# Performance work log

Measured on AMD Instinct MI355X. Metric: run time of the kernel, lower is better.

The kernel has to match this reference:

```python
import jax, jax.numpy as jnp
import numpy as np

B, L, H = 16, 2048, 768
V, D = 30000, 64


def setup_inputs() -> dict:
    key = jax.random.key(0)
    k1, k2, k3, k4 = jax.random.split(key, 4)
    bert_x = jax.random.normal(k1, (B, L, H), dtype=jnp.float32)
    x = jax.random.randint(k2, (B, L), 0, V, dtype=jnp.int64)
    ae = jax.random.normal(k3, (V, D), dtype=jnp.float32)
    w = jax.random.normal(k4, (D, D), dtype=jnp.float32)
    return {"bert_x": bert_x, "x": x, "ae": ae, "w": w}


def reference(bert_x, x, ae, w):
    # E[b,i] = ae[x[b,i]]  -> [B, L, D]
    E = ae[x]
    # fac[b,i,j] = E[b,i] @ w @ E[b,j]   (bilinear pairwise score)
    scores = jnp.einsum('bid,de,bje->bij', E, w, E)
    Lseq = bert_x.shape[1]
    i = jnp.arange(Lseq, dtype=bert_x.dtype)[:, None]
    j = jnp.arange(Lseq, dtype=bert_x.dtype)[None, :]
    # strictly-causal weight (i+1)/(j+1) for i < j, zero elsewhere
    coef = jnp.where(i < j, (i + 1.0) / (j + 1.0), 0.0).astype(bert_x.dtype)
    # res[:, j] = bert_x[:, j] + sum_{i<j} bert_x[:, i] * coef[i,j] * fac[b,i,j]
    res = bert_x + jnp.einsum('bij,bih->bjh', scores * coef, bert_x)
    return res
```

## Files before the change

kernel.cpp:

```cpp
#include <hip/hip_runtime.h>

#define Bb 16
#define Ll 2048
#define Hh 768
#define Dd 64
#define Cc 64
#define HC 64
#define NT (Hh / HC)
#define NCH (Ll / Cc)
#define PSEG 16
#define CPS (NCH / PSEG)
#define NHT (HC / 16)

typedef __attribute__((ext_vector_type(8))) short bf16x8;
typedef __attribute__((ext_vector_type(4))) float f32x4;

__device__ __forceinline__ short f2bf(float f) {
  union { float f; unsigned u; } c;
  c.f = f;
  unsigned r = (c.u + 0x7FFFu + ((c.u >> 16) & 1u)) >> 16;
  return (short)r;
}
__device__ __forceinline__ unsigned pack2(float a, float b) {
  return (unsigned)(unsigned short)f2bf(a) | ((unsigned)(unsigned short)f2bf(b) << 16);
}

__device__ __forceinline__ void sync_lds() {
  asm volatile("s_waitcnt lgkmcnt(0)\n\ts_barrier" ::: "memory");
}

__global__ __launch_bounds__(256) void prep_kernel(const int* __restrict__ x,
                                                   const float* __restrict__ ae,
                                                   const float* __restrict__ w,
                                                   short* __restrict__ Eg,
                                                   short* __restrict__ FTg,
                                                   short* __restrict__ scTg) {
  const int tid = threadIdx.x;
  const int wv = tid >> 6, lane = tid & 63, quad = lane >> 4, lq = lane & 15;
  const int b = blockIdx.x >> 5, ch = blockIdx.x & 31;
  const size_t gb = (size_t)blockIdx.x * 4096;
  __shared__ short sE[64 * 64];
  __shared__ short sWT[64 * 64];
  __shared__ short sF[64 * 64];

  {
    const int i = tid >> 2, seg = tid & 3;
    const int idx = x[b * Ll + ch * Cc + i];
    const float4* aer = (const float4*)(ae + (size_t)idx * Dd) + seg * 4;
    float4 ev[4];
#pragma unroll
    for (int q = 0; q < 4; ++q) ev[q] = aer[q];
    uint4 pA, pB;
    pA.x = pack2(ev[0].x, ev[0].y); pA.y = pack2(ev[0].z, ev[0].w);
    pA.z = pack2(ev[1].x, ev[1].y); pA.w = pack2(ev[1].z, ev[1].w);
    pB.x = pack2(ev[2].x, ev[2].y); pB.y = pack2(ev[2].z, ev[2].w);
    pB.z = pack2(ev[3].x, ev[3].y); pB.w = pack2(ev[3].z, ev[3].w);
    *(uint4*)&sE[i * 64 + (((2 * seg) ^ (i & 7)) << 3)] = pA;
    *(uint4*)&sE[i * 64 + (((2 * seg + 1) ^ (i & 7)) << 3)] = pB;
    *(uint4*)(Eg + gb + i * 64 + seg * 16) = pA;
    *(uint4*)(Eg + gb + i * 64 + seg * 16 + 8) = pB;
    const float4* wr = (const float4*)w;
#pragma unroll
    for (int q = 0; q < 4; ++q) {
      const int fl = q * 256 + tid;
      const int d = fl >> 4, es = (fl & 15) * 4;
      const float4 v = wr[fl];
      const float vv[4] = {v.x, v.y, v.z, v.w};
#pragma unroll
      for (int c = 0; c < 4; ++c) {
        const int e = es + c;
        sWT[e * 64 + (((d >> 3) ^ (e & 7)) << 3) + (d & 7)] = f2bf(vv[c]);
      }
    }
  }
  __syncthreads();

  const int rm = wv * 16 + lq;
  bf16x8 aE[2], aW[2];
#pragma unroll
  for (int ks = 0; ks < 2; ++ks) {
    const int blk = ((ks * 4 + quad) ^ (rm & 7)) << 3;
    aE[ks] = *(const bf16x8*)&sE[rm * 64 + blk];
    aW[ks] = *(const bf16x8*)&sWT[rm * 64 + blk];
  }

#pragma unroll
  for (int nt = 0; nt < 4; ++nt) {
    const int rn = nt * 16 + lq;
    f32x4 accF = {}, accT = {};
#pragma unroll
    for (int ks = 0; ks < 2; ++ks) {
      const int blk = ((ks * 4 + quad) ^ (rn & 7)) << 3;
      const bf16x8 bW = *(const bf16x8*)&sWT[rn * 64 + blk];
      const bf16x8 bE = *(const bf16x8*)&sE[rn * 64 + blk];
      accF = __builtin_amdgcn_mfma_f32_16x16x32_bf16(aE[ks], bW, accF, 0, 0, 0);
      accT = __builtin_amdgcn_mfma_f32_16x16x32_bf16(aW[ks], bE, accT, 0, 0, 0);
    }
#pragma unroll
    for (int r = 0; r < 4; ++r) {
      const int i = wv * 16 + quad * 4 + r;
      const int e = nt * 16 + lq;
      sF[i * 64 + (((e >> 3) ^ (i & 7)) << 3) + (e & 7)] = f2bf(accF[r]);
      const int e2 = wv * 16 + quad * 4 + r;
      const int i2 = nt * 16 + lq;
      FTg[gb + e2 * 64 + i2] = f2bf(accT[r]);
    }
  }
  __syncthreads();

#pragma unroll
  for (int nt = 0; nt < 4; ++nt) {
    const int rn = nt * 16 + lq;
    f32x4 acc = {};
#pragma unroll
    for (int ks = 0; ks < 2; ++ks) {
      const int blk = ((ks * 4 + quad) ^ (rn & 7)) << 3;
      const bf16x8 bF = *(const bf16x8*)&sF[rn * 64 + blk];
      acc = __builtin_amdgcn_mfma_f32_16x16x32_bf16(aE[ks], bF, acc, 0, 0, 0);
    }
#pragma unroll
    for (int r = 0; r < 4; ++r) {
      const int j = wv * 16 + quad * 4 + r;
      const int i = nt * 16 + lq;
      scTg[gb + j * 64 + i] = f2bf(i < j ? acc[r] : 0.f);
    }
  }
}

__global__ __launch_bounds__(256) void state_kernel(const float* __restrict__ bx,
                                                    const short* __restrict__ FTg,
                                                    float* __restrict__ Sg) {
  const int id = blockIdx.x;
  const int t12 = id >> 3;
  const int tile = t12 % NT;
  const int g = ((t12 / NT) << 3) | (id & 7);
  const int b = g / (PSEG - 1), seg = g % (PSEG - 1);
  const int tid = threadIdx.x;
  const int w = tid >> 6, lane = tid & 63, quad = lane >> 4, lq = lane & 15;
  const int ip = tid & 31, hg = tid >> 5;
  const int rj = w * 16 + lq;

  __shared__ short sGT[2][HC * 64];

  f32x4 accS[NHT] = {};
  float4 rGa[2], rGb[2];
  bf16x8 bD[2];

  auto load_G = [&](int ch) {
    const float* xr = bx + ((size_t)(b * Ll) + ch * Cc + 2 * ip) * Hh + tile * HC + hg * 8;
    rGa[0] = *(const float4*)(xr);
    rGa[1] = *(const float4*)(xr + 4);
    rGb[0] = *(const float4*)(xr + Hh);
    rGb[1] = *(const float4*)(xr + Hh + 4);
  };
  auto load_D = [&](int ch) {
    const size_t tb = (size_t)(b * NCH + ch) * 4096;
#pragma unroll
    for (int ks = 0; ks < 2; ++ks)
      bD[ks] = *(const bf16x8*)(FTg + tb + rj * 64 + (ks * 4 + quad) * 8);
  };

  load_G(seg * CPS);
  load_D(seg * CPS);

#pragma unroll
  for (int c = 0; c < CPS; ++c) {
    const int ch = seg * CPS + c;
    const int cur = c & 1;
    const int p0 = ch * Cc;
    {
      const float s0 = (float)(p0 + 2 * ip + 1), s1 = (float)(p0 + 2 * ip + 2);
      const float A[8] = {rGa[0].x, rGa[0].y, rGa[0].z, rGa[0].w,
                          rGa[1].x, rGa[1].y, rGa[1].z, rGa[1].w};
      const float Bv[8] = {rGb[0].x, rGb[0].y, rGb[0].z, rGb[0].w,
                           rGb[1].x, rGb[1].y, rGb[1].z, rGb[1].w};
#pragma unroll
      for (int e = 0; e < 8; ++e) {
        const int h = hg * 8 + e;
        const int sa = h * 64 + (((ip >> 2) ^ (h & 7)) << 3) + 2 * (ip & 3);
        *(unsigned*)&sGT[cur][sa] = pack2(A[e] * s0, Bv[e] * s1);
      }
    }
    if (c + 1 < CPS) load_G(ch + 1);
    sync_lds();
#pragma unroll
    for (int ht = 0; ht < NHT; ++ht) {
      const int rh = ht * 16 + lq;
#pragma unroll
      for (int ks = 0; ks < 2; ++ks) {
        const int blk = ((ks * 4 + quad) ^ (rh & 7)) << 3;
        const bf16x8 gv = *(const bf16x8*)&sGT[cur][rh * 64 + blk];
        accS[ht] = __builtin_amdgcn_mfma_f32_16x16x32_bf16(gv, bD[ks], accS[ht], 0, 0, 0);
      }
    }
    if (c + 1 < CPS) load_D(ch + 1);
  }

  float* Sr = Sg + (size_t)(b * (PSEG - 1) + seg) * (Hh * Dd);
#pragma unroll
  for (int ht = 0; ht < NHT; ++ht)
#pragma unroll
    for (int r = 0; r < 4; ++r) {
      const int h = tile * HC + ht * 16 + quad * 4 + r;
      Sr[h * 64 + w * 16 + lq] = accS[ht][r];
    }
}

__global__ __launch_bounds__(256) void prefix_kernel(float* __restrict__ Sg) {
  const int b = blockIdx.x / 48;
  const int v = (blockIdx.x % 48) * 256 + threadIdx.x;
  float4* base = (float4*)(Sg + (size_t)b * (PSEG - 1) * (Hh * Dd)) + v;
  const int stride = Hh * Dd / 4;
  float4 va[PSEG - 1];
#pragma unroll
  for (int s = 0; s < PSEG - 1; ++s) va[s] = base[s * stride];
  float4 acc = va[0];
#pragma unroll
  for (int s = 1; s < PSEG - 1; ++s) {
    acc.x += va[s].x; acc.y += va[s].y; acc.z += va[s].z; acc.w += va[s].w;
    base[s * stride] = acc;
  }
}

__global__ __launch_bounds__(256) void scan_kernel(const float* __restrict__ bx,
                                                   const short* __restrict__ Eg,
                                                   const short* __restrict__ FTg,
                                                   const short* __restrict__ scTg,
                                                   const float* __restrict__ Sg,
                                                   float* __restrict__ out) {
  const int id = blockIdx.x;
  const int t12 = id >> 3;
  const int tile = t12 % NT;
  const int g = ((t12 / NT) << 3) | (id & 7);
  const int b = g >> 4, seg = g & 15;
  const int tid = threadIdx.x;
  const int w = tid >> 6, lane = tid & 63, quad = lane >> 4, lq = lane & 15;
  const int ip = tid & 31, hg = tid >> 5;
  const int rj = w * 16 + lq;

  __shared__ short sGT[2][HC * 64];
  __shared__ short sST[2][HC * 64];

  f32x4 accS[NHT] = {};
  bf16x8 aC1[2], aC2[2], bD[2];
  float4 rGa[2], rGb[2];

  auto load_G = [&](int ch) {
    const float* xr = bx + ((size_t)(b * Ll) + ch * Cc + 2 * ip) * Hh + tile * HC + hg * 8;
    rGa[0] = *(const float4*)(xr);
    rGa[1] = *(const float4*)(xr + 4);
    rGb[0] = *(const float4*)(xr + Hh);
    rGb[1] = *(const float4*)(xr + Hh + 4);
  };
  auto load_frag = [&](int ch) {
    const size_t tb = (size_t)(b * NCH + ch) * 4096;
#pragma unroll
    for (int ks = 0; ks < 2; ++ks) {
      const int o = rj * 64 + (ks * 4 + quad) * 8;
      aC1[ks] = *(const bf16x8*)(scTg + tb + o);
      aC2[ks] = *(const bf16x8*)(Eg + tb + o);
      bD[ks]  = *(const bf16x8*)(FTg + tb + o);
    }
  };

  load_G(seg * CPS);
  load_frag(seg * CPS);

  if (seg > 0) {
    const float* Pr = Sg + (size_t)(b * (PSEG - 1) + (seg - 1)) * (Hh * Dd);
#pragma unroll
    for (int ht = 0; ht < NHT; ++ht)
#pragma unroll
      for (int r = 0; r < 4; ++r) {
        const int h = tile * HC + ht * 16 + quad * 4 + r;
        accS[ht][r] = Pr[h * 64 + w * 16 + lq];
      }
  }

#pragma unroll
  for (int c = 0; c < CPS; ++c) {
    const int ch = seg * CPS + c;
    const int cur = c & 1;
    const int p0 = ch * Cc;
    {
      const float s0 = (float)(p0 + 2 * ip + 1), s1 = (float)(p0 + 2 * ip + 2);
      const float A[8] = {rGa[0].x, rGa[0].y, rGa[0].z, rGa[0].w,
                          rGa[1].x, rGa[1].y, rGa[1].z, rGa[1].w};
      const float Bv[8] = {rGb[0].x, rGb[0].y, rGb[0].z, rGb[0].w,
                           rGb[1].x, rGb[1].y, rGb[1].z, rGb[1].w};
#pragma unroll
      for (int e = 0; e < 8; ++e) {
        const int h = hg * 8 + e;
        const int sa = h * 64 + (((ip >> 2) ^ (h & 7)) << 3) + 2 * (ip & 3);
        *(unsigned*)&sGT[cur][sa] = pack2(A[e] * s0, Bv[e] * s1);
      }
    }
#pragma unroll
    for (int ht = 0; ht < NHT; ++ht)
#pragma unroll
      for (int r = 0; r < 4; ++r) {
        const int h = ht * 16 + quad * 4 + r;
        const int d = w * 16 + lq;
        sST[cur][h * 64 + (((d >> 3) ^ (h & 7)) << 3) + (d & 7)] = f2bf(accS[ht][r]);
      }
    if (c + 1 < CPS) load_G(ch + 1);
    sync_lds();

    f32x4 accO[NHT] = {};
#pragma unroll
    for (int ht = 0; ht < NHT; ++ht) {
      const int rh = ht * 16 + lq;
#pragma unroll
      for (int ks = 0; ks < 2; ++ks) {
        const int blk = ((ks * 4 + quad) ^ (rh & 7)) << 3;
        const bf16x8 gv = *(const bf16x8*)&sGT[cur][rh * 64 + blk];
        const bf16x8 st = *(const bf16x8*)&sST[cur][rh * 64 + blk];
        accO[ht] = __builtin_amdgcn_mfma_f32_16x16x32_bf16(aC1[ks], gv, accO[ht], 0, 0, 0);
        accO[ht] = __builtin_amdgcn_mfma_f32_16x16x32_bf16(aC2[ks], st, accO[ht], 0, 0, 0);
        accS[ht] = __builtin_amdgcn_mfma_f32_16x16x32_bf16(gv, bD[ks], accS[ht], 0, 0, 0);
      }
    }
    if (c + 1 < CPS) load_frag(ch + 1);

#pragma unroll
    for (int ht = 0; ht < NHT; ++ht)
#pragma unroll
      for (int r = 0; r < 4; ++r) {
        const int gj = p0 + w * 16 + quad * 4 + r;
        const size_t off = ((size_t)(b * Ll) + gj) * Hh + tile * HC + ht * 16 + lq;
        out[off] = bx[off] + accO[ht][r] * (1.0f / (float)(gj + 1));
      }
  }
}

extern "C" void kernel_launch(void* const* d_in, const int* in_sizes, int n_in,
                              void* d_out, int out_size, void* d_ws, size_t ws_size,
                              hipStream_t stream) {
  (void)in_sizes; (void)n_in; (void)out_size; (void)ws_size;
  const float* bx = (const float*)d_in[0];
  const int* x = (const int*)d_in[1];
  const float* ae = (const float*)d_in[2];
  const float* w = (const float*)d_in[3];
  float* out = (float*)d_out;
  short* Eg = (short*)d_ws;
  short* FTg = Eg + (size_t)512 * 4096;
  short* scTg = FTg + (size_t)512 * 4096;
  float* Sg = (float*)(scTg + (size_t)512 * 4096);

  prep_kernel<<<Bb * NCH, 256, 0, stream>>>(x, ae, w, Eg, FTg, scTg);
  state_kernel<<<NT * Bb * (PSEG - 1), 256, 0, stream>>>(bx, FTg, Sg);
  prefix_kernel<<<Bb * 48, 256, 0, stream>>>(Sg);
  scan_kernel<<<NT * Bb * PSEG, 256, 0, stream>>>(bx, Eg, FTg, scTg, Sg, out);
}
```

Measured before the change: 295.3 us.

## Compute per-chunk states in prep and prefix-sum all chunks for parallel scan

Removes the separate state kernel. The prep kernel now computes each chunk's 768x64 state contribution, stored as bf16, for every chunk. A prefix kernel turns these into exclusive prefix sums across all 32 chunks. The scan kernel then handles each chunk independently with no sequential carry, which raises the block count and drops the in-block recurrence. The cost is extra global traffic for writing and rereading the per-chunk bf16 states, plus some precision loss from storing the prefix states in bf16.

```diff
diff --git a/kernel.cpp b/kernel.cpp
--- a/kernel.cpp
+++ b/kernel.cpp
@@ -8,9 +8,7 @@
 #define HC 64
 #define NT (Hh / HC)
 #define NCH (Ll / Cc)
-#define PSEG 16
-#define CPS (NCH / PSEG)
-#define NHT (HC / 16)
+#define NPASS (Hh / 64)
 
 typedef __attribute__((ext_vector_type(8))) short bf16x8;
 typedef __attribute__((ext_vector_type(4))) float f32x4;
@@ -24,6 +22,11 @@
 __device__ __forceinline__ unsigned pack2(float a, float b) {
   return (unsigned)(unsigned short)f2bf(a) | ((unsigned)(unsigned short)f2bf(b) << 16);
 }
+__device__ __forceinline__ float bf2f(unsigned short s) {
+  union { unsigned u; float f; } c;
+  c.u = ((unsigned)s) << 16;
+  return c.f;
+}
 
 __device__ __forceinline__ void sync_lds() {
   asm volatile("s_waitcnt lgkmcnt(0)\n\ts_barrier" ::: "memory");
@@ -32,9 +35,10 @@
 __global__ __launch_bounds__(256) void prep_kernel(const int* __restrict__ x,
                                                    const float* __restrict__ ae,
                                                    const float* __restrict__ w,
+                                                   const float* __restrict__ bx,
                                                    short* __restrict__ Eg,
-                                                   short* __restrict__ FTg,
-                                                   short* __restrict__ scTg) {
+                                                   short* __restrict__ scTg,
+                                                   short* __restrict__ Sch) {
   const int tid = threadIdx.x;
   const int wv = tid >> 6, lane = tid & 63, quad = lane >> 4, lq = lane & 15;
   const int b = blockIdx.x >> 5, ch = blockIdx.x & 31;
@@ -42,6 +46,8 @@
   __shared__ short sE[64 * 64];
   __shared__ short sWT[64 * 64];
   __shared__ short sF[64 * 64];
+  __shared__ short sFT[64 * 64];
+  __shared__ short sGT[2][64 * 64];
 
   {
     const int i = tid >> 2, seg = tid & 3;
@@ -101,12 +107,23 @@
       const int i = wv * 16 + quad * 4 + r;
       const int e = nt * 16 + lq;
       sF[i * 64 + (((e >> 3) ^ (i & 7)) << 3) + (e & 7)] = f2bf(accF[r]);
-      const int e2 = wv * 16 + quad * 4 + r;
+      const int d2 = wv * 16 + quad * 4 + r;
       const int i2 = nt * 16 + lq;
-      FTg[gb + e2 * 64 + i2] = f2bf(accT[r]);
+      sFT[d2 * 64 + (((i2 >> 3) ^ (d2 & 7)) << 3) + (i2 & 7)] = f2bf(accT[r]);
     }
   }
   __syncthreads();
+
+  const int ip = tid & 31, hg = tid >> 5;
+  float4 rGa[2], rGb[2];
+  auto load_G = [&](int p) {
+    const float* xr = bx + ((size_t)(b * Ll) + ch * Cc + 2 * ip) * Hh + p * 64 + hg * 8;
+    rGa[0] = *(const float4*)(xr);
+    rGa[1] = *(const float4*)(xr + 4);
+    rGb[0] = *(const float4*)(xr + Hh);
+    rGb[1] = *(const float4*)(xr + Hh + 4);
+  };
+  load_G(0);
 
 #pragma unroll
   for (int nt = 0; nt < 4; ++nt) {
@@ -125,211 +142,158 @@
       scTg[gb + j * 64 + i] = f2bf(i < j ? acc[r] : 0.f);
     }
   }
-}
-
-__global__ __launch_bounds__(256) void state_kernel(const float* __restrict__ bx,
-                                                    const short* __restrict__ FTg,
-                                                    float* __restrict__ Sg) {
-  const int id = blockIdx.x;
-  const int t12 = id >> 3;
-  const int tile = t12 % NT;
-  const int g = ((t12 / NT) << 3) | (id & 7);
-  const int b = g / (PSEG - 1), seg = g % (PSEG - 1);
+
+  bf16x8 bFT[4][2];
+#pragma unroll
+  for (int nt = 0; nt < 4; ++nt) {
+    const int rn = nt * 16 + lq;
+#pragma unroll
+    for (int ks = 0; ks < 2; ++ks) {
+      const int blk = ((ks * 4 + quad) ^ (rn & 7)) << 3;
+      bFT[nt][ks] = *(const bf16x8*)&sFT[rn * 64 + blk];
+    }
+  }
+
+  short* So = Sch + (size_t)blockIdx.x * (Hh * Dd);
+#pragma unroll 2
+  for (int p = 0; p < NPASS; ++p) {
+    const int cur = p & 1;
+    {
+      const float s0 = (float)(ch * Cc + 2 * ip + 1), s1 = (float)(ch * Cc + 2 * ip + 2);
+      const float A[8] = {rGa[0].x, rGa[0].y, rGa[0].z, rGa[0].w,
+                          rGa[1].x, rGa[1].y, rGa[1].z, rGa[1].w};
+      const float Bv[8] = {rGb[0].x, rGb[0].y, rGb[0].z, rGb[0].w,
+                           rGb[1].x, rGb[1].y, rGb[1].z, rGb[1].w};
+#pragma unroll
+      for (int e = 0; e < 8; ++e) {
+        const int hl = hg * 8 + e;
+        const int sa = hl * 64 + (((ip >> 2) ^ (hl & 7)) << 3) + 2 * (ip & 3);
+        *(unsigned*)&sGT[cur][sa] = pack2(A[e] * s0, Bv[e] * s1);
+      }
+    }
+    if (p + 1 < NPASS) load_G(p + 1);
+    sync_lds();
+    bf16x8 aG[2];
+#pragma unroll
+    for (int ks = 0; ks < 2; ++ks) {
+      const int blk = ((ks * 4 + quad) ^ (rm & 7)) << 3;
+      aG[ks] = *(const bf16x8*)&sGT[cur][rm * 64 + blk];
+    }
+#pragma unroll
+    for (int nt = 0; nt < 4; ++nt) {
+      f32x4 acc = {};
+#pragma unroll
+      for (int ks = 0; ks < 2; ++ks)
+        acc = __builtin_amdgcn_mfma_f32_16x16x32_bf16(aG[ks], bFT[nt][ks], acc, 0, 0, 0);
+#pragma unroll
+      for (int r = 0; r < 4; ++r) {
+        const int h = p * 64 + wv * 16 + quad * 4 + r;
+        So[h * 64 + nt * 16 + lq] = f2bf(acc[r]);
+      }
+    }
+  }
+}
+
+__global__ __launch_bounds__(256) void prefix_kernel(short* __restrict__ Sch) {
+  const int b = blockIdx.x / 48;
+  const int v = (blockIdx.x % 48) * 256 + threadIdx.x;
+  uint2* base = (uint2*)(Sch + (size_t)b * NCH * (Hh * Dd)) + v;
+  const int stride = Hh * Dd / 4;
+  uint2 va[NCH];
+#pragma unroll
+  for (int s = 0; s < NCH; ++s) va[s] = base[s * stride];
+  float4 acc = {0.f, 0.f, 0.f, 0.f};
+#pragma unroll
+  for (int s = 0; s < NCH; ++s) {
+    uint2 o;
+    o.x = pack2(acc.x, acc.y);
+    o.y = pack2(acc.z, acc.w);
+    base[s * stride] = o;
+    acc.x += bf2f((unsigned short)(va[s].x & 0xffffu));
+    acc.y += bf2f((unsigned short)(va[s].x >> 16));
+    acc.z += bf2f((unsigned short)(va[s].y & 0xffffu));
+    acc.w += bf2f((unsigned short)(va[s].y >> 16));
+  }
+}
+
+__global__ __launch_bounds__(256) void scan_kernel(const float* __restrict__ bx,
+                                                   const short* __restrict__ Eg,
+                                                   const short* __restrict__ scTg,
+                                                   const short* __restrict__ STg,
+                                                   float* __restrict__ out) {
+  const int s = blockIdx.x;
+  const int tile = s >> 9;
+  const int bc = s & 511;
+  const int b = bc >> 5, ch = bc & 31;
   const int tid = threadIdx.x;
   const int w = tid >> 6, lane = tid & 63, quad = lane >> 4, lq = lane & 15;
   const int ip = tid & 31, hg = tid >> 5;
   const int rj = w * 16 + lq;
 
-  __shared__ short sGT[2][HC * 64];
-
-  f32x4 accS[NHT] = {};
+  __shared__ short sGT[64 * 64];
+
   float4 rGa[2], rGb[2];
-  bf16x8 bD[2];
-
-  auto load_G = [&](int ch) {
+  {
     const float* xr = bx + ((size_t)(b * Ll) + ch * Cc + 2 * ip) * Hh + tile * HC + hg * 8;
     rGa[0] = *(const float4*)(xr);
     rGa[1] = *(const float4*)(xr + 4);
     rGb[0] = *(const float4*)(xr + Hh);
     rGb[1] = *(const float4*)(xr + Hh + 4);
-  };
-  auto load_D = [&](int ch) {
-    const size_t tb = (size_t)(b * NCH + ch) * 4096;
-#pragma unroll
-    for (int ks = 0; ks < 2; ++ks)
-      bD[ks] = *(const bf16x8*)(FTg + tb + rj * 64 + (ks * 4 + quad) * 8);
-  };
-
-  load_G(seg * CPS);
-  load_D(seg * CPS);
-
-#pragma unroll
-  for (int c = 0; c < CPS; ++c) {
-    const int ch = seg * CPS + c;
-    const int cur = c & 1;
-    const int p0 = ch * Cc;
-    {
-      const float s0 = (float)(p0 + 2 * ip + 1), s1 = (float)(p0 + 2 * ip + 2);
-      const float A[8] = {rGa[0].x, rGa[0].y, rGa[0].z, rGa[0].w,
-                          rGa[1].x, rGa[1].y, rGa[1].z, rGa[1].w};
-      const float Bv[8] = {rGb[0].x, rGb[0].y, rGb[0].z, rGb[0].w,
-                           rGb[1].x, rGb[1].y, rGb[1].z, rGb[1].w};
-#pragma unroll
-      for (int e = 0; e < 8; ++e) {
-        const int h = hg * 8 + e;
-        const int sa = h * 64 + (((ip >> 2) ^ (h & 7)) << 3) + 2 * (ip & 3);
-        *(unsigned*)&sGT[cur][sa] = pack2(A[e] * s0, Bv[e] * s1);
-      }
-    }
-    if (c + 1 < CPS) load_G(ch + 1);
-    sync_lds();
-#pragma unroll
-    for (int ht = 0; ht < NHT; ++ht) {
-      const int rh = ht * 16 + lq;
-#pragma unroll
-      for (int ks = 0; ks < 2; ++ks) {
-        const int blk = ((ks * 4 + quad) ^ (rh & 7)) << 3;
-        const bf16x8 gv = *(const bf16x8*)&sGT[cur][rh * 64 + blk];
-        accS[ht] = __builtin_amdgcn_mfma_f32_16x16x32_bf16(gv, bD[ks], accS[ht], 0, 0, 0);
-      }
-    }
-    if (c + 1 < CPS) load_D(ch + 1);
-  }
-
-  float* Sr = Sg + (size_t)(b * (PSEG - 1) + seg) * (Hh * Dd);
-#pragma unroll
-  for (int ht = 0; ht < NHT; ++ht)
-#pragma unroll
-    for (int r = 0; r < 4; ++r) {
-      const int h = tile * HC + ht * 16 + quad * 4 + r;
-      Sr[h * 64 + w * 16 + lq] = accS[ht][r];
-    }
-}
-
-__global__ __launch_bounds__(256) void prefix_kernel(float* __restrict__ Sg) {
-  const int b = blockIdx.x / 48;
-  const int v = (blockIdx.x % 48) * 256 + threadIdx.x;
-  float4* base = (float4*)(Sg + (size_t)b * (PSEG - 1) * (Hh * Dd)) + v;
-  const int stride = Hh * Dd / 4;
-  float4 va[PSEG - 1];
-#pragma unroll
-  for (int s = 0; s < PSEG - 1; ++s) va[s] = base[s * stride];
-  float4 acc = va[0];
-#pragma unroll
-  for (int s = 1; s < PSEG - 1; ++s) {
-    acc.x += va[s].x; acc.y += va[s].y; acc.z += va[s].z; acc.w += va[s].w;
-    base[s * stride] = acc;
-  }
-}
-
-__global__ __launch_bounds__(256) void scan_kernel(const float* __restrict__ bx,
-                                                   const short* __restrict__ Eg,
-                                                   const short* __restrict__ FTg,
-                                                   const short* __restrict__ scTg,
-                                                   const float* __restrict__ Sg,
-                                                   float* __restrict__ out) {
-  const int id = blockIdx.x;
-  const int t12 = id >> 3;
-  const int tile = t12 % NT;
-  const int g = ((t12 / NT) << 3) | (id & 7);
-  const int b = g >> 4, seg = g & 15;
-  const int tid = threadIdx.x;
-  const int w = tid >> 6, lane = tid & 63, quad = lane >> 4, lq = lane & 15;
-  const int ip = tid & 31, hg = tid >> 5;
-  const int rj = w * 16 + lq;
-
-  __shared__ short sGT[2][HC * 64];
-  __shared__ short sST[2][HC * 64];
-
-  f32x4 accS[NHT] = {};
-  bf16x8 aC1[2], aC2[2], bD[2];
-  float4 rGa[2], rGb[2];
-
-  auto load_G = [&](int ch) {
-    const float* xr = bx + ((size_t)(b * Ll) + ch * Cc + 2 * ip) * Hh + tile * HC + hg * 8;
-    rGa[0] = *(const float4*)(xr);
-    rGa[1] = *(const float4*)(xr + 4);
-    rGb[0] = *(const float4*)(xr + Hh);
-    rGb[1] = *(const float4*)(xr + Hh + 4);
-  };
-  auto load_frag = [&](int ch) {
-    const size_t tb = (size_t)(b * NCH + ch) * 4096;
+  }
+  bf16x8 aC1[2], aC2[2];
+  {
+    const size_t tb = (size_t)bc * 4096;
 #pragma unroll
     for (int ks = 0; ks < 2; ++ks) {
       const int o = rj * 64 + (ks * 4 + quad) * 8;
       aC1[ks] = *(const bf16x8*)(scTg + tb + o);
       aC2[ks] = *(const bf16x8*)(Eg + tb + o);
-      bD[ks]  = *(const bf16x8*)(FTg + tb + o);
-    }
-  };
-
-  load_G(seg * CPS);
-  load_frag(seg * CPS);
-
-  if (seg > 0) {
-    const float* Pr = Sg + (size_t)(b * (PSEG - 1) + (seg - 1)) * (Hh * Dd);
-#pragma unroll
-    for (int ht = 0; ht < NHT; ++ht)
-#pragma unroll
-      for (int r = 0; r < 4; ++r) {
-        const int h = tile * HC + ht * 16 + quad * 4 + r;
-        accS[ht][r] = Pr[h * 64 + w * 16 + lq];
-      }
-  }
-
-#pragma unroll
-  for (int c = 0; c < CPS; ++c) {
-    const int ch = seg * CPS + c;
-    const int cur = c & 1;
-    const int p0 = ch * Cc;
-    {
-      const float s0 = (float)(p0 + 2 * ip + 1), s1 = (float)(p0 + 2 * ip + 2);
-      const float A[8] = {rGa[0].x, rGa[0].y, rGa[0].z, rGa[0].w,
-                          rGa[1].x, rGa[1].y, rGa[1].z, rGa[1].w};
-      const float Bv[8] = {rGb[0].x, rGb[0].y, rGb[0].z, rGb[0].w,
-                           rGb[1].x, rGb[1].y, rGb[1].z, rGb[1].w};
-#pragma unroll
-      for (int e = 0; e < 8; ++e) {
-        const int h = hg * 8 + e;
-        const int sa = h * 64 + (((ip >> 2) ^ (h & 7)) << 3) + 2 * (ip & 3);
-        *(unsigned*)&sGT[cur][sa] = pack2(A[e] * s0, Bv[e] * s1);
-      }
-    }
-#pragma unroll
-    for (int ht = 0; ht < NHT; ++ht)
-#pragma unroll
-      for (int r = 0; r < 4; ++r) {
-        const int h = ht * 16 + quad * 4 + r;
-        const int d = w * 16 + lq;
-        sST[cur][h * 64 + (((d >> 3) ^ (h & 7)) << 3) + (d & 7)] = f2bf(accS[ht][r]);
-      }
-    if (c + 1 < CPS) load_G(ch + 1);
-    sync_lds();
-
-    f32x4 accO[NHT] = {};
-#pragma unroll
-    for (int ht = 0; ht < NHT; ++ht) {
-      const int rh = ht * 16 + lq;
-#pragma unroll
-      for (int ks = 0; ks < 2; ++ks) {
-        const int blk = ((ks * 4 + quad) ^ (rh & 7)) << 3;
-        const bf16x8 gv = *(const bf16x8*)&sGT[cur][rh * 64 + blk];
-        const bf16x8 st = *(const bf16x8*)&sST[cur][rh * 64 + blk];
-        accO[ht] = __builtin_amdgcn_mfma_f32_16x16x32_bf16(aC1[ks], gv, accO[ht], 0, 0, 0);
-        accO[ht] = __builtin_amdgcn_mfma_f32_16x16x32_bf16(aC2[ks], st, accO[ht], 0, 0, 0);
-        accS[ht] = __builtin_amdgcn_mfma_f32_16x16x32_bf16(gv, bD[ks], accS[ht], 0, 0, 0);
-      }
-    }
-    if (c + 1 < CPS) load_frag(ch + 1);
-
-#pragma unroll
-    for (int ht = 0; ht < NHT; ++ht)
-#pragma unroll
-      for (int r = 0; r < 4; ++r) {
-        const int gj = p0 + w * 16 + quad * 4 + r;
-        const size_t off = ((size_t)(b * Ll) + gj) * Hh + tile * HC + ht * 16 + lq;
-        out[off] = bx[off] + accO[ht][r] * (1.0f / (float)(gj + 1));
-      }
+    }
+  }
+  bf16x8 stF[4][2];
+  {
+    const short* Sp = STg + (size_t)bc * (Hh * Dd);
+#pragma unroll
+    for (int ht = 0; ht < 4; ++ht) {
+      const int h = tile * HC + ht * 16 + lq;
+#pragma unroll
+      for (int ks = 0; ks < 2; ++ks)
+        stF[ht][ks] = *(const bf16x8*)(Sp + h * 64 + (ks * 4 + quad) * 8);
+    }
+  }
+
+  {
+    const float s0 = (float)(ch * Cc + 2 * ip + 1), s1 = (float)(ch * Cc + 2 * ip + 2);
+    const float A[8] = {rGa[0].x, rGa[0].y, rGa[0].z, rGa[0].w,
+                        rGa[1].x, rGa[1].y, rGa[1].z, rGa[1].w};
+    const float Bv[8] = {rGb[0].x, rGb[0].y, rGb[0].z, rGb[0].w,
+                         rGb[1].x, rGb[1].y, rGb[1].z, rGb[1].w};
+#pragma unroll
+    for (int e = 0; e < 8; ++e) {
+      const int hl = hg * 8 + e;
+      const int sa = hl * 64 + (((ip >> 2) ^ (hl & 7)) << 3) + 2 * (ip & 3);
+      *(unsigned*)&sGT[sa] = pack2(A[e] * s0, Bv[e] * s1);
+    }
+  }
+  sync_lds();
+
+#pragma unroll
+  for (int ht = 0; ht < 4; ++ht) {
+    const int rh = ht * 16 + lq;
+    f32x4 accO = {};
+#pragma unroll
+    for (int ks = 0; ks < 2; ++ks) {
+      const int blk = ((ks * 4 + quad) ^ (rh & 7)) << 3;
+      const bf16x8 gv = *(const bf16x8*)&sGT[rh * 64 + blk];
+      accO = __builtin_amdgcn_mfma_f32_16x16x32_bf16(aC1[ks], gv, accO, 0, 0, 0);
+      accO = __builtin_amdgcn_mfma_f32_16x16x32_bf16(aC2[ks], stF[ht][ks], accO, 0, 0, 0);
+    }
+#pragma unroll
+    for (int r = 0; r < 4; ++r) {
+      const int gj = ch * Cc + w * 16 + quad * 4 + r;
+      const size_t off = ((size_t)(b * Ll) + gj) * Hh + tile * HC + ht * 16 + lq;
+      out[off] = bx[off] + accO[r] * (1.0f / (float)(gj + 1));
+    }
   }
 }
 
@@ -343,12 +307,10 @@
   const float* w = (const float*)d_in[3];
   float* out = (float*)d_out;
   short* Eg = (short*)d_ws;
-  short* FTg = Eg + (size_t)512 * 4096;
-  short* scTg = FTg + (size_t)512 * 4096;
-  float* Sg = (float*)(scTg + (size_t)512 * 4096);
-
-  prep_kernel<<<Bb * NCH, 256, 0, stream>>>(x, ae, w, Eg, FTg, scTg);
-  state_kernel<<<NT * Bb * (PSEG - 1), 256, 0, stream>>>(bx, FTg, Sg);
-  prefix_kernel<<<Bb * 48, 256, 0, stream>>>(Sg);
-  scan_kernel<<<NT * Bb * PSEG, 256, 0, stream>>>(bx, Eg, FTg, scTg, Sg, out);
-}
+  short* scTg = Eg + (size_t)512 * 4096;
+  short* Sch = scTg + (size_t)512 * 4096;
+
+  prep_kernel<<<Bb * NCH, 256, 0, stream>>>(x, ae, w, bx, Eg, scTg, Sch);
+  prefix_kernel<<<Bb * 48, 256, 0, stream>>>(Sch);
+  scan_kernel<<<NT * Bb * NCH, 256, 0, stream>>>(bx, Eg, scTg, Sch, out);
+}
```

Result: faster. 265.9 us (-9.9%).
